# Kernel tuning notes

Hardware: AMD Instinct MI355X
Metric: run time of the kernel (lower is better)

The kernel has to match this reference:

```python
import jax, jax.numpy as jnp
import numpy as np

N_NODES = 100000
N_EDGES = 1600000
D_IN = 64
D_OUT = 64
K_PLUS = 3
ALPHA = 0.5
EXPONENT = -0.25


def _dir_norm_edge_weights(row, col, n, exponent):
    # directed_norm: D_out^exp A D_in^exp, zero-degree -> 0 weight
    ones = jnp.ones(row.shape[0], dtype=jnp.float32)
    out_deg = jax.ops.segment_sum(ones, row, num_segments=n)
    in_deg = jax.ops.segment_sum(ones, col, num_segments=n)
    out_inv = jnp.where(out_deg > 0, jnp.power(jnp.maximum(out_deg, 1.0), exponent), 0.0)
    in_inv = jnp.where(in_deg > 0, jnp.power(jnp.maximum(in_deg, 1.0), exponent), 0.0)
    return out_inv[row] * in_inv[col]


def _spmm(w, x, out_idx, gather_idx, n):
    # y[out_idx] += w * x[gather_idx]
    return jax.ops.segment_sum(w[:, None] * x[gather_idx], out_idx, num_segments=n)


def setup_inputs() -> dict:
    key = jax.random.key(0)
    ks = jax.random.split(key, 7)
    x_real = jax.random.normal(ks[0], (N_NODES, D_IN), dtype=jnp.float32)
    x_imag = jax.random.normal(ks[1], (N_NODES, D_IN), dtype=jnp.float32)
    edge_index = jax.random.randint(ks[2], (2, N_EDGES), 0, N_NODES, dtype=jnp.int32)
    s = 1.0 / np.sqrt(D_IN)
    W_real = jax.random.normal(ks[3], (K_PLUS, D_OUT, D_IN), dtype=jnp.float32) * s
    b_real = jax.random.normal(ks[4], (K_PLUS, D_OUT), dtype=jnp.float32) * s
    W_imag = jax.random.normal(ks[5], (K_PLUS, D_OUT, D_IN), dtype=jnp.float32) * s
    b_imag = jax.random.normal(ks[6], (K_PLUS, D_OUT), dtype=jnp.float32) * s
    return {"x_real": x_real, "x_imag": x_imag, "edge_index": edge_index,
            "W_real": W_real, "b_real": b_real, "W_imag": W_imag, "b_imag": b_imag}


def reference(x_real, x_imag, edge_index, W_real, b_real, W_imag, b_imag):
    n = x_real.shape[0]
    row, col = edge_index[0], edge_index[1]
    # adj_norm edge weights; adj_t_norm weights are identical scalars per edge
    # (in/out degrees swap under transpose), only the scatter direction differs.
    w = _dir_norm_edge_weights(row, col, n, EXPONENT)

    y_real = _spmm(w, x_real, row, col, n)    # adj_norm @ x_real
    y_imag = _spmm(w, x_imag, row, col, n)    # adj_norm @ x_imag
    y_real_t = _spmm(w, x_real, col, row, n)  # adj_t_norm @ x_real
    y_imag_t = _spmm(w, x_imag, col, row, n)  # adj_t_norm @ x_imag

    def lin_r(y):  # [K, N, O] per-order real linear
        return jnp.einsum('nd,kod->kno', y, W_real) + b_real[:, None, :]

    def lin_i(y):
        return jnp.einsum('nd,kod->kno', y, W_imag) + b_imag[:, None, :]

    coeffs = (0.5 ** jnp.arange(K_PLUS, dtype=jnp.float32))[:, None, None]  # exp penalty, i=0 -> 1

    lr_yr, li_yr = lin_r(y_real), lin_i(y_real)
    lr_yi, li_yi = lin_r(y_imag), lin_i(y_imag)
    lr_yrt, li_yrt = lin_r(y_real_t), lin_i(y_real_t)
    lr_yit, li_yit = lin_r(y_imag_t), lin_i(y_imag_t)

    sum_real_s2d = jnp.sum((lr_yr - li_yi) * coeffs, axis=0)
    sum_imag_s2d = jnp.sum((li_yr + lr_yi) * coeffs, axis=0)
    sum_real_d2s = jnp.sum((lr_yrt - li_yit) * coeffs, axis=0)
    # NOTE: faithful to original source, which uses y_real (not y_real_t) here.
    sum_imag_d2s = jnp.sum((li_yr + lr_yit) * coeffs, axis=0)

    total_real = ALPHA * sum_real_s2d + (1.0 - ALPHA) * sum_real_d2s
    total_imag = ALPHA * sum_imag_s2d + (1.0 - ALPHA) * sum_imag_d2s
    return total_real, total_imag
```

## Files before the change

kernel.cpp:

```cpp
#include <hip/hip_runtime.h>
#include <hip/hip_fp16.h>


constexpr int D = 64;
constexpr int SB = 256;
constexpr int G1 = 256;

typedef _Float16 f16x8 __attribute__((ext_vector_type(8)));
typedef float f32x4 __attribute__((ext_vector_type(4)));

__device__ __forceinline__ float2 h2_to_f2(uint p) {
  __half2 h = *(__half2*)&p;
  return __half22float2(h);
}


__global__ __launch_bounds__(256) void part_count(
    const int* __restrict__ row, const int* __restrict__ col,
    int* __restrict__ hout, int* __restrict__ hin, int E, int NBUK, int CH) {
  __shared__ int ho[256], hi_[256];
  int t = threadIdx.x, g = blockIdx.x;
  ho[t] = 0;
  hi_[t] = 0;
  __syncthreads();
  int e0 = g * CH, e1 = min(E, e0 + CH);
  for (int e = e0 + t; e < e1; e += 256) {
    atomicAdd(&ho[row[e] >> 9], 1);
    atomicAdd(&hi_[col[e] >> 9], 1);
  }
  __syncthreads();
  if (t < NBUK) {
    hout[t * G1 + g] = ho[t];
    hin[t * G1 + g] = hi_[t];
  }
}

__global__ __launch_bounds__(256) void part_scatter(
    const int* __restrict__ row, const int* __restrict__ col,
    const int* __restrict__ hout, const int* __restrict__ hin,
    uint* __restrict__ pout, uint* __restrict__ pin, int E, int NBUK, int CH) {
  __shared__ int co[256], ci[256];
  int t = threadIdx.x, g = blockIdx.x;
  if (t < NBUK) {
    co[t] = hout[t * G1 + g];
    ci[t] = hin[t * G1 + g];
  }
  __syncthreads();
  int e0 = g * CH, e1 = min(E, e0 + CH);
  for (int e = e0 + t; e < e1; e += 256) {
    int r = row[e], c = col[e];
    int po = atomicAdd(&co[r >> 9], 1);
    pout[po] = ((uint)(r & 511) << 17) | (uint)c;
    int pi = atomicAdd(&ci[c >> 9], 1);
    pin[pi] = ((uint)(c & 511) << 17) | (uint)r;
  }
}

__global__ __launch_bounds__(256) void bucket_degree(
    const uint* __restrict__ pout, const uint* __restrict__ pin,
    const int* __restrict__ hout, const int* __restrict__ hin,
    int* __restrict__ deg_out, int* __restrict__ deg_in, int E, int NBUK, int N) {
  const uint* p = blockIdx.y ? pin : pout;
  const int* h = blockIdx.y ? hin : hout;
  int* deg = blockIdx.y ? deg_in : deg_out;
  __shared__ int ld[512];
  int t = threadIdx.x, b = blockIdx.x;
  ld[t] = 0;
  ld[t + 256] = 0;
  __syncthreads();
  int s = h[b * G1];
  int e = (b + 1 < NBUK) ? h[(b + 1) * G1] : E;
  for (int j = s + t; j < e; j += 256) atomicAdd(&ld[p[j] >> 17], 1);
  __syncthreads();
  int n0 = (b << 9) + t;
  if (n0 < N) deg[n0] = ld[t];
  if (n0 + 256 < N) deg[n0 + 256] = ld[t + 256];
}

__global__ __launch_bounds__(256) void bucket_fill(
    const uint* __restrict__ pout, const uint* __restrict__ pin,
    const int* __restrict__ hout, const int* __restrict__ hin,
    const int* __restrict__ ofs_out, const int* __restrict__ ofs_in,
    uint* __restrict__ idx_out, uint* __restrict__ idx_in, int E, int NBUK, int N) {
  const uint* p = blockIdx.y ? pin : pout;
  const int* h = blockIdx.y ? hin : hout;
  const int* ofs = blockIdx.y ? ofs_in : ofs_out;
  uint* idx = blockIdx.y ? idx_in : idx_out;
  __shared__ int cur[512];
  int t = threadIdx.x, b = blockIdx.x;
  int n0 = (b << 9) + t;
  cur[t] = (n0 < N) ? ofs[n0] : 0;
  cur[t + 256] = (n0 + 256 < N) ? ofs[n0 + 256] : 0;
  __syncthreads();
  int s = h[b * G1];
  int e = (b + 1 < NBUK) ? h[(b + 1) * G1] : E;
  for (int j = s + t; j < e; j += 256) {
    uint pk = p[j];
    int pos = atomicAdd(&cur[pk >> 17], 1);
    idx[pos] = pk & 0x1FFFFu;
  }
}


__global__ __launch_bounds__(SB) void bsum_kernel(
    const int* __restrict__ a0, const int* __restrict__ a1,
    int* __restrict__ bsum, int n, int NB) {
  const int* a = blockIdx.y ? a1 : a0;
  int i = blockIdx.x * SB + threadIdx.x;
  int d = (i < n) ? a[i] : 0;
#pragma unroll
  for (int m = 1; m < 64; m <<= 1) d += __shfl_xor(d, m);
  __shared__ int ws[SB / 64];
  if ((threadIdx.x & 63) == 0) ws[threadIdx.x >> 6] = d;
  __syncthreads();
  if (threadIdx.x == 0) {
    int s = 0;
#pragma unroll
    for (int w = 0; w < SB / 64; ++w) s += ws[w];
    bsum[blockIdx.y * NB + blockIdx.x] = s;
  }
}

__global__ __launch_bounds__(1024) void bscan_kernel(int* __restrict__ bsum, int NB) {
  __shared__ int s0[1024], s1[1024];
  int t = threadIdx.x;
  int o0 = (t < NB) ? bsum[t] : 0;
  int o1 = (t < NB) ? bsum[NB + t] : 0;
  s0[t] = o0;
  s1[t] = o1;
  __syncthreads();
  for (int off = 1; off < 1024; off <<= 1) {
    int v0 = (t >= off) ? s0[t - off] : 0;
    int v1 = (t >= off) ? s1[t - off] : 0;
    __syncthreads();
    s0[t] += v0;
    s1[t] += v1;
    __syncthreads();
  }
  if (t < NB) {
    bsum[t] = s0[t] - o0;
    bsum[NB + t] = s1[t] - o1;
  }
}

__global__ __launch_bounds__(SB) void gfin_kernel(
    int* __restrict__ h0, int* __restrict__ h1,
    const int* __restrict__ bsum, int n, int NB) {
  int* h = blockIdx.y ? h1 : h0;
  int base = bsum[blockIdx.y * NB + blockIdx.x];
  int lane = threadIdx.x & 63, wv = threadIdx.x >> 6;
  int i = blockIdx.x * SB + threadIdx.x;
  int d = (i < n) ? h[i] : 0;
  int sc = d;
#pragma unroll
  for (int off = 1; off < 64; off <<= 1) {
    int v = __shfl_up(sc, off);
    if (lane >= off) sc += v;
  }
  __shared__ int ws[SB / 64];
  if (lane == 63) ws[wv] = sc;
  __syncthreads();
  int wbase = 0;
#pragma unroll
  for (int w = 0; w < SB / 64; ++w)
    if (w < wv) wbase += ws[w];
  if (i < n) h[i] = base + wbase + (sc - d);
}

__global__ __launch_bounds__(SB) void sfin_kernel(
    const int* __restrict__ deg_out, const int* __restrict__ deg_in,
    const int* __restrict__ bsum,
    int* __restrict__ ofs_out, int* __restrict__ ofs_in,
    float* __restrict__ inv_out, float* __restrict__ inv_in, int N, int NB) {
  const int* deg = blockIdx.y ? deg_in : deg_out;
  int* ofs = blockIdx.y ? ofs_in : ofs_out;
  float* inv = blockIdx.y ? inv_in : inv_out;
  int base = bsum[blockIdx.y * NB + blockIdx.x];
  int lane = threadIdx.x & 63, wv = threadIdx.x >> 6;
  int i = blockIdx.x * SB + threadIdx.x;
  int d = (i < N) ? deg[i] : 0;
  int sc = d;
#pragma unroll
  for (int off = 1; off < 64; off <<= 1) {
    int v = __shfl_up(sc, off);
    if (lane >= off) sc += v;
  }
  __shared__ int ws[SB / 64];
  if (lane == 63) ws[wv] = sc;
  __syncthreads();
  int wbase = 0;
#pragma unroll
  for (int w = 0; w < SB / 64; ++w)
    if (w < wv) wbase += ws[w];
  if (i < N) {
    ofs[i] = base + wbase + (sc - d);
    inv[i] = d > 0 ? rsqrtf(sqrtf((float)d)) : 0.0f;
  }
  if (i == N - 1) ofs[N] = base + wbase + sc;
}


__global__ void pack_kernel(const float* __restrict__ xr, const float* __restrict__ xi,
                            const float* __restrict__ inv_out, const float* __restrict__ inv_in,
                            uint* __restrict__ xout_p, uint* __restrict__ xin_p, int total4) {
  int i = blockIdx.x * blockDim.x + threadIdx.x;
  if (i < total4) {
    int n = i >> 4;
    float4 a = ((const float4*)xr)[i];
    float4 b = ((const float4*)xi)[i];
    float io = inv_out[n], ii = inv_in[n];
    __half2 h;
    uint4 o, p;
    h = __floats2half2_rn(io * a.x, io * b.x); o.x = *(uint*)&h;
    h = __floats2half2_rn(io * a.y, io * b.y); o.y = *(uint*)&h;
    h = __floats2half2_rn(io * a.z, io * b.z); o.z = *(uint*)&h;
    h = __floats2half2_rn(io * a.w, io * b.w); o.w = *(uint*)&h;
    h = __floats2half2_rn(ii * a.x, ii * b.x); p.x = *(uint*)&h;
    h = __floats2half2_rn(ii * a.y, ii * b.y); p.y = *(uint*)&h;
    h = __floats2half2_rn(ii * a.z, ii * b.z); p.z = *(uint*)&h;
    h = __floats2half2_rn(ii * a.w, ii * b.w); p.w = *(uint*)&h;
    ((uint4*)xout_p)[i] = o;
    ((uint4*)xin_p)[i] = p;
  }
}

__global__ void weights_kernel(const float* __restrict__ Wr, const float* __restrict__ br,
                               const float* __restrict__ Wi, const float* __restrict__ bi,
                               uint* __restrict__ Wh, float* __restrict__ cR,
                               float* __restrict__ cI) {
  int i = blockIdx.x * blockDim.x + threadIdx.x;
  if (i < 4096) {
    int o = i >> 6, d = i & 63;
    float wr = Wr[i] + 0.5f * Wr[4096 + i] + 0.25f * Wr[8192 + i];
    float wi = Wi[i] + 0.5f * Wi[4096 + i] + 0.25f * Wi[8192 + i];
    __half2 h = __floats2half2_rn(wr, wi);
    Wh[d * 64 + o] = *(uint*)&h;
    if (i < 64) {
      float brv = br[i] + 0.5f * br[64 + i] + 0.25f * br[128 + i];
      float biv = bi[i] + 0.5f * bi[64 + i] + 0.25f * bi[128 + i];
      cR[i] = brv - biv;
      cI[i] = brv + biv;
    }
  }
}

__global__ __launch_bounds__(256) void bprep_kernel(
    const uint* __restrict__ Wh, uint4* __restrict__ Bfrag) {
  int t = blockIdx.x * blockDim.x + threadIdx.x;
  if (t >= 2048) return;
  int lane = t & 63, fr = t >> 6;
  int mat = fr >> 4, kt = (fr >> 2) & 3, nt = fr & 3;
  int o = (lane & 15) + 16 * nt;
  int k0 = 8 * (lane >> 4) + 32 * kt;
  uint wbits[4];
#pragma unroll
  for (int jj = 0; jj < 4; ++jj) {
    float v[2];
#pragma unroll
    for (int s = 0; s < 2; ++s) {
      int k = k0 + 2 * jj + s;
      uint wv_ = Wh[(k & 63) * 64 + o];
      float2 wrwi = h2_to_f2(wv_);
      v[s] = (k < 64) ? wrwi.x : (mat ? wrwi.y : -wrwi.y);
    }
    __half2 hh = __floats2half2_rn(v[0], v[1]);
    wbits[jj] = *(uint*)&hh;
  }
  Bfrag[t] = make_uint4(wbits[0], wbits[1], wbits[2], wbits[3]);
}

__global__ __launch_bounds__(256) void gather_kernel(
    const uint4* __restrict__ xout4, const uint4* __restrict__ xin4,
    const uint* __restrict__ idx_out, const uint* __restrict__ idx_in,
    const int* __restrict__ ofs_out, const int* __restrict__ ofs_in,
    const float* __restrict__ inv_out, const float* __restrict__ inv_in,
    uint* __restrict__ Apack, int N) {
  int wv = threadIdx.x >> 6;
  int lane = threadIdx.x & 63;
  int sub = lane >> 4;
  int q = lane & 15;
  int wid = blockIdx.x * 4 + wv;
  int nw = gridDim.x * 4;
  for (int n = wid; n < N; n += nw) {
    float4 u1 = {0, 0, 0, 0}, s1 = {0, 0, 0, 0};
    float4 v2 = {0, 0, 0, 0}, s2 = {0, 0, 0, 0};
#define ACC(P, U, S)                                          \
  {                                                           \
    float2 a0 = h2_to_f2((P).x), a1 = h2_to_f2((P).y);        \
    float2 a2 = h2_to_f2((P).z), a3 = h2_to_f2((P).w);        \
    U.x += a0.x; S.x += a0.y; U.y += a1.x; S.y += a1.y;       \
    U.z += a2.x; S.z += a2.y; U.w += a3.x; S.w += a3.y;       \
  }
    {
      int lo = ofs_out[n], hi = ofs_out[n + 1];
      int len8 = (hi - lo) & ~7;
      int j = lo;
      for (; j < lo + len8; j += 8) {
        uint4 p0 = xin4[(size_t)idx_out[j + sub] * 16 + q];
        uint4 p1 = xin4[(size_t)idx_out[j + 4 + sub] * 16 + q];
        ACC(p0, u1, s1);
        ACC(p1, u1, s1);
      }
      for (; j < hi; j += 4) {
        if (j + sub < hi) {
          uint4 p0 = xin4[(size_t)idx_out[j + sub] * 16 + q];
          ACC(p0, u1, s1);
        }
      }
    }
    {
      int lo = ofs_in[n], hi = ofs_in[n + 1];
      int len8 = (hi - lo) & ~7;
      int j = lo;
      for (; j < lo + len8; j += 8) {
        uint4 p0 = xout4[(size_t)idx_in[j + sub] * 16 + q];
        uint4 p1 = xout4[(size_t)idx_in[j + 4 + sub] * 16 + q];
        ACC(p0, v2, s2);
        ACC(p1, v2, s2);
      }
      for (; j < hi; j += 4) {
        if (j + sub < hi) {
          uint4 p0 = xout4[(size_t)idx_in[j + sub] * 16 + q];
          ACC(p0, v2, s2);
        }
      }
    }
#undef ACC
#pragma unroll
    for (int m = 16; m < 64; m <<= 1) {
      u1.x += __shfl_xor(u1.x, m); u1.y += __shfl_xor(u1.y, m);
      u1.z += __shfl_xor(u1.z, m); u1.w += __shfl_xor(u1.w, m);
      s1.x += __shfl_xor(s1.x, m); s1.y += __shfl_xor(s1.y, m);
      s1.z += __shfl_xor(s1.z, m); s1.w += __shfl_xor(s1.w, m);
      v2.x += __shfl_xor(v2.x, m); v2.y += __shfl_xor(v2.y, m);
      v2.z += __shfl_xor(v2.z, m); v2.w += __shfl_xor(v2.w, m);
      s2.x += __shfl_xor(s2.x, m); s2.y += __shfl_xor(s2.y, m);
      s2.z += __shfl_xor(s2.z, m); s2.w += __shfl_xor(s2.w, m);
    }
    if (sub == 0) {
      float io = inv_out[n], ii = inv_in[n];
      float4 uu = make_float4(io * u1.x, io * u1.y, io * u1.z, io * u1.w);
      float4 vv = make_float4(ii * v2.x, ii * v2.y, ii * v2.z, ii * v2.w);
      float4 ss = make_float4(io * s1.x + ii * s2.x, io * s1.y + ii * s2.y,
                              io * s1.z + ii * s2.z, io * s1.w + ii * s2.w);
      uint* base = Apack + (size_t)n * 96 + 2 * q;
      __half2 h;
      uint2 w;
      h = __floats2half2_rn(0.5f * (uu.x + vv.x), 0.5f * (uu.y + vv.y)); w.x = *(uint*)&h;
      h = __floats2half2_rn(0.5f * (uu.z + vv.z), 0.5f * (uu.w + vv.w)); w.y = *(uint*)&h;
      *(uint2*)base = w;
      h = __floats2half2_rn(0.5f * ss.x, 0.5f * ss.y); w.x = *(uint*)&h;
      h = __floats2half2_rn(0.5f * ss.z, 0.5f * ss.w); w.y = *(uint*)&h;
      *(uint2*)(base + 32) = w;
      h = __floats2half2_rn(uu.x, uu.y); w.x = *(uint*)&h;
      h = __floats2half2_rn(uu.z, uu.w); w.y = *(uint*)&h;
      *(uint2*)(base + 64) = w;
    }
  }
}

__global__ __launch_bounds__(256) void gemm_kernel(
    const ushort* __restrict__ Apack, const uint4* __restrict__ Bfrag,
    const float* __restrict__ cR, const float* __restrict__ cI,
    float* __restrict__ out_real, float* __restrict__ out_imag, int N) {
  __shared__ uint4 sB[2048];
  for (int i = threadIdx.x; i < 2048; i += 256) sB[i] = Bfrag[i];
  __syncthreads();
  int lane = threadIdx.x & 63, wv = threadIdx.x >> 6;
  int l15 = lane & 15, l4 = lane >> 4;
  float bR[4], bI[4];
#pragma unroll
  for (int nt = 0; nt < 4; ++nt) {
    bR[nt] = cR[l15 + 16 * nt];
    bI[nt] = cI[l15 + 16 * nt];
  }
  int tiles = (N + 15) >> 4;
  int gw = blockIdx.x * 4 + wv, nw = gridDim.x * 4;
  for (int tt = gw; tt < tiles; tt += nw) {
    int n0 = tt << 4;
    int arow = min(n0 + l15, N - 1);
    const ushort* ap = Apack + (size_t)arow * 192 + 8 * l4;
    f16x8 a[6];
#pragma unroll
    for (int kt = 0; kt < 6; ++kt) a[kt] = *(const f16x8*)(ap + 32 * kt);
    f32x4 cr[4], ci[4];
#pragma unroll
    for (int nt = 0; nt < 4; ++nt) {
      cr[nt] = (f32x4){0.f, 0.f, 0.f, 0.f};
      ci[nt] = (f32x4){0.f, 0.f, 0.f, 0.f};
    }
#pragma unroll
    for (int kt = 0; kt < 4; ++kt) {
#pragma unroll
      for (int nt = 0; nt < 4; ++nt) {
        f16x8 b0 = *(const f16x8*)&sB[(kt * 4 + nt) * 64 + lane];
        cr[nt] = __builtin_amdgcn_mfma_f32_16x16x32_f16(a[kt], b0, cr[nt], 0, 0, 0);
        f16x8 b1 = *(const f16x8*)&sB[(16 + kt * 4 + nt) * 64 + lane];
        ci[nt] = __builtin_amdgcn_mfma_f32_16x16x32_f16(a[kt + 2], b1, ci[nt], 0, 0, 0);
      }
    }
#pragma unroll
    for (int nt = 0; nt < 4; ++nt) {
#pragma unroll
      for (int r = 0; r < 4; ++r) {
        int node = n0 + 4 * l4 + r;
        if (node < N) {
          out_real[(size_t)node * 64 + l15 + 16 * nt] = cr[nt][r] + bR[nt];
          out_imag[(size_t)node * 64 + l15 + 16 * nt] = ci[nt][r] + bI[nt];
        }
      }
    }
  }
}

extern "C" void kernel_launch(void* const* d_in, const int* in_sizes, int n_in,
                              void* d_out, int out_size, void* d_ws, size_t ws_size,
                              hipStream_t stream) {
  const float* x_real = (const float*)d_in[0];
  const float* x_imag = (const float*)d_in[1];
  const int* edge = (const int*)d_in[2];
  const float* W_real = (const float*)d_in[3];
  const float* b_real = (const float*)d_in[4];
  const float* W_imag = (const float*)d_in[5];
  const float* b_imag = (const float*)d_in[6];

  const int N = in_sizes[0] / D;
  const int E = in_sizes[2] / 2;
  const int* row = edge;
  const int* col = edge + E;

  const int NBUK = (N + 511) >> 9;
  const int CH = (E + G1 - 1) / G1;
  const int L = NBUK * G1;
  const int GB = (L + SB - 1) / SB;
  const int NB = (N + SB - 1) / SB;

  uint* xout_p   = (uint*)d_ws;
  uint* xin_p    = xout_p + (size_t)N * D;
  uint* idx_out  = xin_p + (size_t)N * D;
  uint* idx_in   = idx_out + E;
  uint* Apack    = idx_in + E;
  uint* pout     = Apack;
  uint* pin      = pout + E;
  uint4* Bfrag   = (uint4*)(Apack + (size_t)N * 96);
  int* hout      = (int*)(Bfrag + 2048);
  int* hin       = hout + L;
  int* gbs       = hin + L;
  int* deg_out   = gbs + 2 * GB;
  int* deg_in    = deg_out + N;
  int* ofs_out   = deg_in + N;
  int* ofs_in    = ofs_out + N + 1;
  float* inv_out = (float*)(ofs_in + N + 1);
  float* inv_in  = inv_out + N;
  uint* Wh       = (uint*)(inv_in + N);
  float* cR      = (float*)(Wh + 4096);
  float* cI      = cR + 64;
  int* bsum      = (int*)(cI + 64);

  float* out_real = (float*)d_out;
  float* out_imag = out_real + (size_t)N * D;

  weights_kernel<<<16, 256, 0, stream>>>(W_real, b_real, W_imag, b_imag, Wh, cR, cI);
  bprep_kernel<<<8, 256, 0, stream>>>(Wh, Bfrag);

  part_count<<<G1, 256, 0, stream>>>(row, col, hout, hin, E, NBUK, CH);
  bsum_kernel<<<dim3(GB, 2), SB, 0, stream>>>(hout, hin, gbs, L, GB);
  bscan_kernel<<<1, 1024, 0, stream>>>(gbs, GB);
  gfin_kernel<<<dim3(GB, 2), SB, 0, stream>>>(hout, hin, gbs, L, GB);
  part_scatter<<<G1, 256, 0, stream>>>(row, col, hout, hin, pout, pin, E, NBUK, CH);

  bucket_degree<<<dim3(NBUK, 2), 256, 0, stream>>>(pout, pin, hout, hin,
                                                   deg_out, deg_in, E, NBUK, N);
  bsum_kernel<<<dim3(NB, 2), SB, 0, stream>>>(deg_out, deg_in, bsum, N, NB);
  bscan_kernel<<<1, 1024, 0, stream>>>(bsum, NB);
  sfin_kernel<<<dim3(NB, 2), SB, 0, stream>>>(deg_out, deg_in, bsum, ofs_out, ofs_in,
                                              inv_out, inv_in, N, NB);

  pack_kernel<<<(N * 16 + 255) / 256, 256, 0, stream>>>(x_real, x_imag, inv_out, inv_in,
                                                        xout_p, xin_p, N * 16);
  bucket_fill<<<dim3(NBUK, 2), 256, 0, stream>>>(pout, pin, hout, hin, ofs_out, ofs_in,
                                                 idx_out, idx_in, E, NBUK, N);
  gather_kernel<<<4096, 256, 0, stream>>>((const uint4*)xout_p, (const uint4*)xin_p,
                                          idx_out, idx_in, ofs_out, ofs_in,
                                          inv_out, inv_in, Apack, N);
  gemm_kernel<<<512, 256, 0, stream>>>((const ushort*)Apack, Bfrag, cR, cI,
                                       out_real, out_imag, N);
}
```

Measured before the change: 348.1 us.

## Store single unscaled fp16 x copy and fold neighbor scale into edge index

Instead of writing two pre-scaled fp16 copies of the interleaved features (one per degree normalization), the pack kernel now writes a single unscaled copy. The neighbor's inverse-degree factor is stored as fp16 in the upper 15 bits of each CSR index entry, and the gather multiplies by it per edge. This halves the packed-feature write and the gather's random-read working set, which should improve cache hit rates. Two weight-prep kernels are also merged into one block using shared memory. The cost is extra per-edge decode and multiply work, a sign-less 15-bit half that truncates the top bit (the scales are positive, so this is fine), and an extra random read of inv in bucket_fill.

```diff
diff --git a/kernel.cpp b/kernel.cpp
--- a/kernel.cpp
+++ b/kernel.cpp
@@ -81,10 +81,12 @@
     const uint* __restrict__ pout, const uint* __restrict__ pin,
     const int* __restrict__ hout, const int* __restrict__ hin,
     const int* __restrict__ ofs_out, const int* __restrict__ ofs_in,
+    const float* __restrict__ inv_out, const float* __restrict__ inv_in,
     uint* __restrict__ idx_out, uint* __restrict__ idx_in, int E, int NBUK, int N) {
   const uint* p = blockIdx.y ? pin : pout;
   const int* h = blockIdx.y ? hin : hout;
   const int* ofs = blockIdx.y ? ofs_in : ofs_out;
+  const float* invnb = blockIdx.y ? inv_out : inv_in;
   uint* idx = blockIdx.y ? idx_in : idx_out;
   __shared__ int cur[512];
   int t = threadIdx.x, b = blockIdx.x;
@@ -96,8 +98,10 @@
   int e = (b + 1 < NBUK) ? h[(b + 1) * G1] : E;
   for (int j = s + t; j < e; j += 256) {
     uint pk = p[j];
+    uint nbr = pk & 0x1FFFFu;
+    uint hb = (uint)__half_as_ushort(__float2half(invnb[nbr]));
     int pos = atomicAdd(&cur[pk >> 17], 1);
-    idx[pos] = pk & 0x1FFFFu;
+    idx[pos] = (hb << 17) | nbr;
   }
 }
 
@@ -201,76 +205,65 @@
 
 
 __global__ void pack_kernel(const float* __restrict__ xr, const float* __restrict__ xi,
-                            const float* __restrict__ inv_out, const float* __restrict__ inv_in,
-                            uint* __restrict__ xout_p, uint* __restrict__ xin_p, int total4) {
+                            uint* __restrict__ xp, int total4) {
   int i = blockIdx.x * blockDim.x + threadIdx.x;
   if (i < total4) {
-    int n = i >> 4;
     float4 a = ((const float4*)xr)[i];
     float4 b = ((const float4*)xi)[i];
-    float io = inv_out[n], ii = inv_in[n];
     __half2 h;
-    uint4 o, p;
-    h = __floats2half2_rn(io * a.x, io * b.x); o.x = *(uint*)&h;
-    h = __floats2half2_rn(io * a.y, io * b.y); o.y = *(uint*)&h;
-    h = __floats2half2_rn(io * a.z, io * b.z); o.z = *(uint*)&h;
-    h = __floats2half2_rn(io * a.w, io * b.w); o.w = *(uint*)&h;
-    h = __floats2half2_rn(ii * a.x, ii * b.x); p.x = *(uint*)&h;
-    h = __floats2half2_rn(ii * a.y, ii * b.y); p.y = *(uint*)&h;
-    h = __floats2half2_rn(ii * a.z, ii * b.z); p.z = *(uint*)&h;
-    h = __floats2half2_rn(ii * a.w, ii * b.w); p.w = *(uint*)&h;
-    ((uint4*)xout_p)[i] = o;
-    ((uint4*)xin_p)[i] = p;
-  }
-}
-
-__global__ void weights_kernel(const float* __restrict__ Wr, const float* __restrict__ br,
-                               const float* __restrict__ Wi, const float* __restrict__ bi,
-                               uint* __restrict__ Wh, float* __restrict__ cR,
-                               float* __restrict__ cI) {
-  int i = blockIdx.x * blockDim.x + threadIdx.x;
-  if (i < 4096) {
+    uint4 o;
+    h = __floats2half2_rn(a.x, b.x); o.x = *(uint*)&h;
+    h = __floats2half2_rn(a.y, b.y); o.y = *(uint*)&h;
+    h = __floats2half2_rn(a.z, b.z); o.z = *(uint*)&h;
+    h = __floats2half2_rn(a.w, b.w); o.w = *(uint*)&h;
+    ((uint4*)xp)[i] = o;
+  }
+}
+
+__global__ __launch_bounds__(1024) void wprep_kernel(
+    const float* __restrict__ Wr, const float* __restrict__ br,
+    const float* __restrict__ Wi, const float* __restrict__ bi,
+    uint4* __restrict__ Bfrag, float* __restrict__ cR, float* __restrict__ cI) {
+  __shared__ uint sWh[4096];
+  int t = threadIdx.x;
+  for (int i = t; i < 4096; i += 1024) {
     int o = i >> 6, d = i & 63;
     float wr = Wr[i] + 0.5f * Wr[4096 + i] + 0.25f * Wr[8192 + i];
     float wi = Wi[i] + 0.5f * Wi[4096 + i] + 0.25f * Wi[8192 + i];
     __half2 h = __floats2half2_rn(wr, wi);
-    Wh[d * 64 + o] = *(uint*)&h;
-    if (i < 64) {
-      float brv = br[i] + 0.5f * br[64 + i] + 0.25f * br[128 + i];
-      float biv = bi[i] + 0.5f * bi[64 + i] + 0.25f * bi[128 + i];
-      cR[i] = brv - biv;
-      cI[i] = brv + biv;
-    }
-  }
-}
-
-__global__ __launch_bounds__(256) void bprep_kernel(
-    const uint* __restrict__ Wh, uint4* __restrict__ Bfrag) {
-  int t = blockIdx.x * blockDim.x + threadIdx.x;
-  if (t >= 2048) return;
-  int lane = t & 63, fr = t >> 6;
-  int mat = fr >> 4, kt = (fr >> 2) & 3, nt = fr & 3;
-  int o = (lane & 15) + 16 * nt;
-  int k0 = 8 * (lane >> 4) + 32 * kt;
-  uint wbits[4];
-#pragma unroll
-  for (int jj = 0; jj < 4; ++jj) {
-    float v[2];
-#pragma unroll
-    for (int s = 0; s < 2; ++s) {
-      int k = k0 + 2 * jj + s;
-      uint wv_ = Wh[(k & 63) * 64 + o];
-      float2 wrwi = h2_to_f2(wv_);
-      v[s] = (k < 64) ? wrwi.x : (mat ? wrwi.y : -wrwi.y);
-    }
-    __half2 hh = __floats2half2_rn(v[0], v[1]);
-    wbits[jj] = *(uint*)&hh;
-  }
-  Bfrag[t] = make_uint4(wbits[0], wbits[1], wbits[2], wbits[3]);
+    sWh[d * 64 + o] = *(uint*)&h;
+  }
+  if (t < 64) {
+    float brv = br[t] + 0.5f * br[64 + t] + 0.25f * br[128 + t];
+    float biv = bi[t] + 0.5f * bi[64 + t] + 0.25f * bi[128 + t];
+    cR[t] = brv - biv;
+    cI[t] = brv + biv;
+  }
+  __syncthreads();
+  for (int tt = t; tt < 2048; tt += 1024) {
+    int lane = tt & 63, fr = tt >> 6;
+    int mat = fr >> 4, kt = (fr >> 2) & 3, nt = fr & 3;
+    int o = (lane & 15) + 16 * nt;
+    int k0 = 8 * (lane >> 4) + 32 * kt;
+    uint wbits[4];
+#pragma unroll
+    for (int jj = 0; jj < 4; ++jj) {
+      float v[2];
+#pragma unroll
+      for (int s = 0; s < 2; ++s) {
+        int k = k0 + 2 * jj + s;
+        float2 wrwi = h2_to_f2(sWh[(k & 63) * 64 + o]);
+        v[s] = (k < 64) ? wrwi.x : (mat ? wrwi.y : -wrwi.y);
+      }
+      __half2 hh = __floats2half2_rn(v[0], v[1]);
+      wbits[jj] = *(uint*)&hh;
+    }
+    Bfrag[tt] = make_uint4(wbits[0], wbits[1], wbits[2], wbits[3]);
+  }
 }
 
 __global__ __launch_bounds__(256) void gather_kernel(
-    const uint4* __restrict__ xout4, const uint4* __restrict__ xin4,
+    const uint4* __restrict__ xp4,
     const uint* __restrict__ idx_out, const uint* __restrict__ idx_in,
     const int* __restrict__ ofs_out, const int* __restrict__ ofs_in,
     const float* __restrict__ inv_out, const float* __restrict__ inv_in,
@@ -284,27 +277,33 @@
   for (int n = wid; n < N; n += nw) {
     float4 u1 = {0, 0, 0, 0}, s1 = {0, 0, 0, 0};
     float4 v2 = {0, 0, 0, 0}, s2 = {0, 0, 0, 0};
-#define ACC(P, U, S)                                          \
-  {                                                           \
-    float2 a0 = h2_to_f2((P).x), a1 = h2_to_f2((P).y);        \
-    float2 a2 = h2_to_f2((P).z), a3 = h2_to_f2((P).w);        \
-    U.x += a0.x; S.x += a0.y; U.y += a1.x; S.y += a1.y;       \
-    U.z += a2.x; S.z += a2.y; U.w += a3.x; S.w += a3.y;       \
-  }
+#define ACC(P, SC, U, S)                                                \
+  {                                                                     \
+    float2 a0 = h2_to_f2((P).x), a1 = h2_to_f2((P).y);                  \
+    float2 a2 = h2_to_f2((P).z), a3 = h2_to_f2((P).w);                  \
+    U.x += SC * a0.x; S.x += SC * a0.y; U.y += SC * a1.x; S.y += SC * a1.y; \
+    U.z += SC * a2.x; S.z += SC * a2.y; U.w += SC * a3.x; S.w += SC * a3.y; \
+  }
+#define DEC(E) __half2float(__ushort_as_half((ushort)((E) >> 17)))
     {
       int lo = ofs_out[n], hi = ofs_out[n + 1];
       int len8 = (hi - lo) & ~7;
       int j = lo;
       for (; j < lo + len8; j += 8) {
-        uint4 p0 = xin4[(size_t)idx_out[j + sub] * 16 + q];
-        uint4 p1 = xin4[(size_t)idx_out[j + 4 + sub] * 16 + q];
-        ACC(p0, u1, s1);
-        ACC(p1, u1, s1);
+        uint e0 = idx_out[j + sub];
+        uint e1 = idx_out[j + 4 + sub];
+        uint4 p0 = xp4[(size_t)(e0 & 0x1FFFFu) * 16 + q];
+        uint4 p1 = xp4[(size_t)(e1 & 0x1FFFFu) * 16 + q];
+        float sc0 = DEC(e0), sc1 = DEC(e1);
+        ACC(p0, sc0, u1, s1);
+        ACC(p1, sc1, u1, s1);
       }
       for (; j < hi; j += 4) {
         if (j + sub < hi) {
-          uint4 p0 = xin4[(size_t)idx_out[j + sub] * 16 + q];
-          ACC(p0, u1, s1);
+          uint e0 = idx_out[j + sub];
+          uint4 p0 = xp4[(size_t)(e0 & 0x1FFFFu) * 16 + q];
+          float sc0 = DEC(e0);
+          ACC(p0, sc0, u1, s1);
         }
       }
     }
@@ -313,19 +312,25 @@
       int len8 = (hi - lo) & ~7;
       int j = lo;
       for (; j < lo + len8; j += 8) {
-        uint4 p0 = xout4[(size_t)idx_in[j + sub] * 16 + q];
-        uint4 p1 = xout4[(size_t)idx_in[j + 4 + sub] * 16 + q];
-        ACC(p0, v2, s2);
-        ACC(p1, v2, s2);
+        uint e0 = idx_in[j + sub];
+        uint e1 = idx_in[j + 4 + sub];
+        uint4 p0 = xp4[(size_t)(e0 & 0x1FFFFu) * 16 + q];
+        uint4 p1 = xp4[(size_t)(e1 & 0x1FFFFu) * 16 + q];
+        float sc0 = DEC(e0), sc1 = DEC(e1);
+        ACC(p0, sc0, v2, s2);
+        ACC(p1, sc1, v2, s2);
       }
       for (; j < hi; j += 4) {
         if (j + sub < hi) {
-          uint4 p0 = xout4[(size_t)idx_in[j + sub] * 16 + q];
-          ACC(p0, v2, s2);
+          uint e0 = idx_in[j + sub];
+          uint4 p0 = xp4[(size_t)(e0 & 0x1FFFFu) * 16 + q];
+          float sc0 = DEC(e0);
+          ACC(p0, sc0, v2, s2);
         }
       }
     }
 #undef ACC
+#undef DEC
 #pragma unroll
     for (int m = 16; m < 64; m <<= 1) {
       u1.x += __shfl_xor(u1.x, m); u1.y += __shfl_xor(u1.y, m);
@@ -435,9 +440,8 @@
   const int GB = (L + SB - 1) / SB;
   const int NB = (N + SB - 1) / SB;
 
-  uint* xout_p   = (uint*)d_ws;
-  uint* xin_p    = xout_p + (size_t)N * D;
-  uint* idx_out  = xin_p + (size_t)N * D;
+  uint* xp       = (uint*)d_ws;
+  uint* idx_out  = xp + (size_t)N * D;
   uint* idx_in   = idx_out + E;
   uint* Apack    = idx_in + E;
   uint* pout     = Apack;
@@ -452,16 +456,16 @@
   int* ofs_in    = ofs_out + N + 1;
   float* inv_out = (float*)(ofs_in + N + 1);
   float* inv_in  = inv_out + N;
-  uint* Wh       = (uint*)(inv_in + N);
-  float* cR      = (float*)(Wh + 4096);
+  float* cR      = inv_in + N;
   float* cI      = cR + 64;
   int* bsum      = (int*)(cI + 64);
 
   float* out_real = (float*)d_out;
   float* out_imag = out_real + (size_t)N * D;
 
-  weights_kernel<<<16, 256, 0, stream>>>(W_real, b_real, W_imag, b_imag, Wh, cR, cI);
-  bprep_kernel<<<8, 256, 0, stream>>>(Wh, Bfrag);
+  wprep_kernel<<<1, 1024, 0, stream>>>(W_real, b_real, W_imag, b_imag, Bfrag, cR, cI);
+
+  pack_kernel<<<(N * 16 + 255) / 256, 256, 0, stream>>>(x_real, x_imag, xp, N * 16);
 
   part_count<<<G1, 256, 0, stream>>>(row, col, hout, hin, E, NBUK, CH);
   bsum_kernel<<<dim3(GB, 2), SB, 0, stream>>>(hout, hin, gbs, L, GB);
@@ -476,13 +480,11 @@
   sfin_kernel<<<dim3(NB, 2), SB, 0, stream>>>(deg_out, deg_in, bsum, ofs_out, ofs_in,
                                               inv_out, inv_in, N, NB);
 
-  pack_kernel<<<(N * 16 + 255) / 256, 256, 0, stream>>>(x_real, x_imag, inv_out, inv_in,
-                                                        xout_p, xin_p, N * 16);
   bucket_fill<<<dim3(NBUK, 2), 256, 0, stream>>>(pout, pin, hout, hin, ofs_out, ofs_in,
-                                                 idx_out, idx_in, E, NBUK, N);
-  gather_kernel<<<4096, 256, 0, stream>>>((const uint4*)xout_p, (const uint4*)xin_p,
-                                          idx_out, idx_in, ofs_out, ofs_in,
-                                          inv_out, inv_in, Apack, N);
+                                                 inv_out, inv_in, idx_out, idx_in,
+                                                 E, NBUK, N);
+  gather_kernel<<<4096, 256, 0, stream>>>((const uint4*)xp, idx_out, idx_in,
+                                          ofs_out, ofs_in, inv_out, inv_in, Apack, N);
   gemm_kernel<<<512, 256, 0, stream>>>((const ushort*)Apack, Bfrag, cR, cI,
                                        out_real, out_imag, N);
 }
```

After: 346.1 us. Within noise of the previous version (-0.6%).
